# Kernel optimization log

Hardware: AMD Instinct MI355X
Metric: run time of the kernel (lower is better)

The kernel has to match this reference:

```python
import jax, jax.numpy as jnp
import numpy as np

E, C, CAP = 16, 256, 4  # experts, channels per expert, capacity expansion

def setup_inputs() -> dict:
    key = jax.random.key(0)
    k1, k2, k3, k4, k5 = jax.random.split(key, 5)
    B, L = 8, 1024
    x = jax.random.normal(k1, (B, E * C, L), dtype=jnp.float32)
    # Conv1d weights (kernel_size=1 squeezed): [out_ch, in_ch_per_group]
    W1 = jax.random.normal(k2, (E * C * CAP, C), dtype=jnp.float32) * (1.0 / np.sqrt(C))
    b1 = jax.random.normal(k3, (E * C * CAP,), dtype=jnp.float32) * 0.01
    W2 = jax.random.normal(k4, (E * C, C * CAP), dtype=jnp.float32) * (1.0 / np.sqrt(C * CAP))
    b2 = jax.random.normal(k5, (E * C,), dtype=jnp.float32) * 0.01
    return {"x": x, "W1": W1, "b1": b1, "W2": W2, "b2": b2}

def reference(x, W1, b1, W2, b2):
    # Grouped 1x1 Conv1d == block-diagonal per-expert matmul over length axis.
    B, CE, L = x.shape
    xr = x.reshape(B, E, C, L)                       # [B,E,C,L]
    W1r = W1.reshape(E, C * CAP, C)                  # [E,F,C], F = C*CAP
    W2r = W2.reshape(E, C, C * CAP)                  # [E,C,F]
    h = jnp.einsum('becl,efc->befl', xr, W1r) + b1.reshape(1, E, C * CAP, 1)
    h = jax.nn.silu(h)                               # [B,E,F,L]
    y = jnp.einsum('befl,ecf->becl', h, W2r) + b2.reshape(1, E, C, 1)
    return y.reshape(B, E * C, L)
```

## Files before the change

### kernel.cpp

```cpp
#include <hip/hip_runtime.h>
#include <hip/hip_bf16.h>
#include <stdint.h>

#define EE 16
#define CC 256
#define FF 1024
#define LL 1024
#define BB 8
#define TL 128
#define FC 32
#define NCH 32
#define HSTR 40

typedef __bf16 bf16x8 __attribute__((ext_vector_type(8)));
typedef __bf16 bf16x4 __attribute__((ext_vector_type(4)));
typedef float  f32x4  __attribute__((ext_vector_type(4)));

__device__ __forceinline__ f32x4 mfma16(bf16x8 a, bf16x8 b, f32x4 c) {
    return __builtin_amdgcn_mfma_f32_16x16x32_bf16(a, b, c, 0, 0, 0);
}

__device__ __forceinline__ void gld_lds16(const __bf16* g, __bf16* l) {
    __builtin_amdgcn_global_load_lds(
        (const __attribute__((address_space(1))) void*)g,
        (__attribute__((address_space(3))) void*)l, 16, 0, 0);
}

__global__ __launch_bounds__(256)
void cvt_both(const float* __restrict__ W1, const float* __restrict__ W2,
              __bf16* __restrict__ ws1, __bf16* __restrict__ ws2)
{
    __shared__ __align__(16) __bf16 ls[8448];
    const int t = threadIdx.x;
    const int bid = blockIdx.x;
    if (bid < 512) {
        const float* src = W1 + (size_t)bid * 8192;
        #pragma unroll
        for (int i = 0; i < 8; ++i) {
            const int p = t + 256 * i;
            const float4 v = *(const float4*)(src + 4 * p);
            const int f = p >> 6, c4 = p & 63;
            const int cg = c4 >> 1, j0 = (c4 & 1) * 4;
            bf16x4 o;
            o[0] = (__bf16)v.x; o[1] = (__bf16)v.y; o[2] = (__bf16)v.z; o[3] = (__bf16)v.w;
            *(bf16x4*)(ls + cg * 264 + f * 8 + j0) = o;
        }
        __syncthreads();
        __bf16* dst = ws1 + (size_t)bid * 8192;
        #pragma unroll
        for (int i = 0; i < 4; ++i) {
            const int G = t + 256 * i;
            const int cg = G >> 5, f = G & 31;
            *(bf16x8*)(dst + (size_t)G * 8) = *(const bf16x8*)(ls + cg * 264 + f * 8);
        }
    } else {
        const int tile = bid - 512;
        const float* src = W2 + (size_t)(tile >> 5) * 262144 + (tile & 31) * 32;
        #pragma unroll
        for (int i = 0; i < 8; ++i) {
            const int u = t + 256 * i;
            const int c = u >> 3, col4 = u & 7;
            const float4 v = *(const float4*)(src + (size_t)c * 1024 + col4 * 4);
            const int fg = col4 >> 1, j0 = (col4 & 1) * 4;
            bf16x4 o;
            o[0] = (__bf16)v.x; o[1] = (__bf16)v.y; o[2] = (__bf16)v.z; o[3] = (__bf16)v.w;
            *(bf16x4*)(ls + fg * 2056 + c * 8 + j0) = o;
        }
        __syncthreads();
        __bf16* dst = ws2 + (size_t)tile * 8192;
        #pragma unroll
        for (int i = 0; i < 4; ++i) {
            const int G = t + 256 * i;
            const int fg = G >> 8, c = G & 255;
            *(bf16x8*)(dst + (size_t)G * 8) = *(const bf16x8*)(ls + fg * 2056 + c * 8);
        }
    }
}

__global__ __launch_bounds__(1024, 4)
void experts_kernel(const float* __restrict__ x,
                    const __bf16* __restrict__ w1ws,
                    const float* __restrict__ b1,
                    const __bf16* __restrict__ w2ws,
                    const float* __restrict__ b2,
                    float* __restrict__ out)
{
    __shared__ __align__(16) __bf16 sW1[3][FC * CC];
    __shared__ __align__(16) __bf16 sW2[3][CC * FC];
    __shared__ __align__(16) __bf16 sH[2][4][32 * HSTR];

    const int tid  = threadIdx.x;
    const int lane = tid & 63;
    const int w    = tid >> 6;
    const int l15  = lane & 15, q4 = lane >> 4;
    const bool prod = (w < 8);
    const int fh   = w & 1;
    const int lw   = (w & 7) >> 1;

    const int bid  = blockIdx.x;
    const int e    = ((bid & 7) << 1) | ((bid >> 3) & 1);
    const int rest = bid >> 4;
    const int bb   = rest & 7;
    const int l0   = (rest >> 3) * TL;
    const int lb   = l0 + 32 * lw;

    const __bf16* w1c = w1ws + (size_t)e * (NCH * FC * CC);
    const __bf16* w2c = w2ws + (size_t)e * (NCH * CC * FC);
    const int slice = w * 512;

    gld_lds16(w1c + 0 * 8192 + slice + lane * 8, &sW1[0][slice]);
    gld_lds16(w2c + 0 * 8192 + slice + lane * 8, &sW2[0][slice]);
    gld_lds16(w1c + 1 * 8192 + slice + lane * 8, &sW1[1][slice]);
    gld_lds16(w2c + 1 * 8192 + slice + lane * 8, &sW2[1][slice]);

    f32x4 st[2][8];
    if (prod) {
        const float* xp = x + ((size_t)(bb * EE + e) * CC) * LL + lb + l15;
        #pragma unroll
        for (int lt = 0; lt < 2; ++lt) {
            #pragma unroll
            for (int ks = 0; ks < 8; ++ks) {
                bf16x8 f;
                #pragma unroll
                for (int u = 0; u < 8; ++u)
                    f[u] = (__bf16)xp[(size_t)(32 * ks + 8 * q4 + u) * LL + 16 * lt];
                st[lt][ks] = __builtin_bit_cast(f32x4, f);
            }
        }
    } else {
        #pragma unroll
        for (int lt = 0; lt < 2; ++lt)
            #pragma unroll
            for (int u = 0; u < 8; ++u) st[lt][u] = f32x4{0.f, 0.f, 0.f, 0.f};
    }

    __syncthreads();

    int rp = 0;
    #pragma unroll 1
    for (int ch = 0; ch <= NCH; ++ch) {
        const int rq = (rp >= 1) ? rp - 1 : 2;

        if (prod) {
            if (ch < NCH) {
                const float4 bv = *(const float4*)(b1 + e * FF + ch * FC + 16 * fh + 4 * q4);
                f32x4 a0 = f32x4{0.f, 0.f, 0.f, 0.f};
                f32x4 a1 = f32x4{0.f, 0.f, 0.f, 0.f};
                const __bf16* a1base = &sW1[rp][(16 * fh + l15) * 8];
                __builtin_amdgcn_s_setprio(1);
                #pragma unroll
                for (int ks = 0; ks < 8; ++ks) {
                    bf16x8 a = *(const bf16x8*)(a1base + (4 * ks + q4) * 256);
                    a0 = mfma16(a, __builtin_bit_cast(bf16x8, st[0][ks]), a0);
                    a1 = mfma16(a, __builtin_bit_cast(bf16x8, st[1][ks]), a1);
                }
                __builtin_amdgcn_s_setprio(0);
                __bf16* hrow = &sH[ch & 1][lw][l15 * HSTR + 16 * fh + 4 * q4];
                bf16x4 hv;
                #pragma unroll
                for (int r = 0; r < 4; ++r) {
                    float v = a0[r] + ((const float*)&bv)[r];
                    hv[r] = (__bf16)(v / (1.0f + __expf(-v)));
                }
                *(bf16x4*)hrow = hv;
                #pragma unroll
                for (int r = 0; r < 4; ++r) {
                    float v = a1[r] + ((const float*)&bv)[r];
                    hv[r] = (__bf16)(v / (1.0f + __expf(-v)));
                }
                *(bf16x4*)(hrow + 16 * HSTR) = hv;
            }
        } else if (ch >= 1) {
            const __bf16* hbase = &sH[(ch & 1) ^ 1][lw][l15 * HSTR + 8 * q4];
            bf16x8 h0 = *(const bf16x8*)(hbase);
            bf16x8 h1 = *(const bf16x8*)(hbase + 16 * HSTR);
            const __bf16* a2base = &sW2[rq][(128 * fh + l15) * 8];
            __builtin_amdgcn_s_setprio(1);
            #pragma unroll
            for (int u = 0; u < 8; ++u) {
                bf16x8 a = *(const bf16x8*)(a2base + (q4 * 256 + 16 * u) * 8);
                st[0][u] = mfma16(a, h0, st[0][u]);
                st[1][u] = mfma16(a, h1, st[1][u]);
            }
            __builtin_amdgcn_s_setprio(0);
        }

        if (ch < NCH) {
            __syncthreads();
            if (ch + 2 < NCH) {
                gld_lds16(w1c + (size_t)(ch + 2) * 8192 + slice + lane * 8, &sW1[rq][slice]);
                gld_lds16(w2c + (size_t)(ch + 2) * 8192 + slice + lane * 8, &sW2[rq][slice]);
            }
        }
        rp = (rp >= 2) ? 0 : rp + 1;
    }

    if (!prod) {
        float* outp = out + ((size_t)(bb * EE + e) * CC) * LL + lb + l15;
        #pragma unroll
        for (int u = 0; u < 8; ++u) {
            const int c0 = 128 * fh + 16 * u + 4 * q4;
            const float4 b2v = *(const float4*)(b2 + e * CC + c0);
            #pragma unroll
            for (int lt = 0; lt < 2; ++lt) {
                #pragma unroll
                for (int r = 0; r < 4; ++r)
                    __builtin_nontemporal_store(
                        st[lt][u][r] + ((const float*)&b2v)[r],
                        outp + (size_t)(c0 + r) * LL + 16 * lt);
            }
        }
    }
}

extern "C" void kernel_launch(void* const* d_in, const int* in_sizes, int n_in,
                              void* d_out, int out_size, void* d_ws, size_t ws_size,
                              hipStream_t stream)
{
    const float* x  = (const float*)d_in[0];
    const float* W1 = (const float*)d_in[1];
    const float* b1 = (const float*)d_in[2];
    const float* W2 = (const float*)d_in[3];
    const float* b2 = (const float*)d_in[4];
    float* out = (float*)d_out;

    const size_t nW1 = (size_t)EE * FF * CC;
    __bf16* w1bf = (__bf16*)d_ws;
    __bf16* w2bf = w1bf + nW1;

    cvt_both<<<dim3(1024), dim3(256), 0, stream>>>(W1, W2, w1bf, w2bf);

    experts_kernel<<<dim3(BB * EE * (LL / TL)), dim3(1024), 0, stream>>>(
        x, w1bf, b1, w2bf, b2, out);
}
```

Before: 455.4 us.

## Read expert weights directly from global memory and halve the L tile

Removes the triple-buffered LDS staging of W1/W2 chunks through global_load_lds. Each wave now loads its MFMA A-fragments straight from global memory, relying on L2 for reuse. The L tile shrinks from 128 to 64 and the block from 1024 to 512 threads, which doubles the grid and cuts LDS use to the small H exchange buffer, allowing more resident blocks. The cost is more global/L2 weight traffic per unit of work, since each block fetches the full expert weights for half as many columns, and weight-load latency is no longer hidden by prefetching. The s_setprio hint is also dropped from the first GEMM.

```diff
diff --git a/kernel.cpp b/kernel.cpp
--- a/kernel.cpp
+++ b/kernel.cpp
@@ -7,7 +7,7 @@
 #define FF 1024
 #define LL 1024
 #define BB 8
-#define TL 128
+#define TL 64
 #define FC 32
 #define NCH 32
 #define HSTR 40
@@ -18,12 +18,6 @@
 
 __device__ __forceinline__ f32x4 mfma16(bf16x8 a, bf16x8 b, f32x4 c) {
     return __builtin_amdgcn_mfma_f32_16x16x32_bf16(a, b, c, 0, 0, 0);
-}
-
-__device__ __forceinline__ void gld_lds16(const __bf16* g, __bf16* l) {
-    __builtin_amdgcn_global_load_lds(
-        (const __attribute__((address_space(1))) void*)g,
-        (__attribute__((address_space(3))) void*)l, 16, 0, 0);
 }
 
 __global__ __launch_bounds__(256)
@@ -77,7 +71,7 @@
     }
 }
 
-__global__ __launch_bounds__(1024, 4)
+__global__ __launch_bounds__(512, 4)
 void experts_kernel(const float* __restrict__ x,
                     const __bf16* __restrict__ w1ws,
                     const float* __restrict__ b1,
@@ -85,17 +79,16 @@
                     const float* __restrict__ b2,
                     float* __restrict__ out)
 {
-    __shared__ __align__(16) __bf16 sW1[3][FC * CC];
-    __shared__ __align__(16) __bf16 sW2[3][CC * FC];
-    __shared__ __align__(16) __bf16 sH[2][4][32 * HSTR];
+    __shared__ __align__(16) __bf16 sH[2][2][32 * HSTR];
 
     const int tid  = threadIdx.x;
     const int lane = tid & 63;
     const int w    = tid >> 6;
     const int l15  = lane & 15, q4 = lane >> 4;
-    const bool prod = (w < 8);
-    const int fh   = w & 1;
-    const int lw   = (w & 7) >> 1;
+    const bool prod = (w < 4);
+    const int wr   = w & 3;
+    const int fh   = wr & 1;
+    const int lw   = wr >> 1;
 
     const int bid  = blockIdx.x;
     const int e    = ((bid & 7) << 1) | ((bid >> 3) & 1);
@@ -104,14 +97,10 @@
     const int l0   = (rest >> 3) * TL;
     const int lb   = l0 + 32 * lw;
 
-    const __bf16* w1c = w1ws + (size_t)e * (NCH * FC * CC);
-    const __bf16* w2c = w2ws + (size_t)e * (NCH * CC * FC);
-    const int slice = w * 512;
-
-    gld_lds16(w1c + 0 * 8192 + slice + lane * 8, &sW1[0][slice]);
-    gld_lds16(w2c + 0 * 8192 + slice + lane * 8, &sW2[0][slice]);
-    gld_lds16(w1c + 1 * 8192 + slice + lane * 8, &sW1[1][slice]);
-    gld_lds16(w2c + 1 * 8192 + slice + lane * 8, &sW2[1][slice]);
+    const __bf16* w1p = w1ws + (size_t)e * (NCH * FC * CC)
+                      + q4 * 256 + (16 * fh + l15) * 8;
+    const __bf16* w2p = w2ws + (size_t)e * (NCH * CC * FC)
+                      + q4 * 2048 + (128 * fh + l15) * 8;
 
     f32x4 st[2][8];
     if (prod) {
@@ -134,27 +123,20 @@
             for (int u = 0; u < 8; ++u) st[lt][u] = f32x4{0.f, 0.f, 0.f, 0.f};
     }
 
-    __syncthreads();
-
-    int rp = 0;
     #pragma unroll 1
     for (int ch = 0; ch <= NCH; ++ch) {
-        const int rq = (rp >= 1) ? rp - 1 : 2;
-
         if (prod) {
             if (ch < NCH) {
                 const float4 bv = *(const float4*)(b1 + e * FF + ch * FC + 16 * fh + 4 * q4);
-                f32x4 a0 = f32x4{0.f, 0.f, 0.f, 0.f};
-                f32x4 a1 = f32x4{0.f, 0.f, 0.f, 0.f};
-                const __bf16* a1base = &sW1[rp][(16 * fh + l15) * 8];
-                __builtin_amdgcn_s_setprio(1);
+                const __bf16* wp = w1p + (size_t)ch * 8192;
+                f32x4 a0 = f32x4{0.f,0.f,0.f,0.f};
+                f32x4 a1 = f32x4{0.f,0.f,0.f,0.f};
                 #pragma unroll
                 for (int ks = 0; ks < 8; ++ks) {
-                    bf16x8 a = *(const bf16x8*)(a1base + (4 * ks + q4) * 256);
+                    bf16x8 a = *(const bf16x8*)(wp + ks * 1024);
                     a0 = mfma16(a, __builtin_bit_cast(bf16x8, st[0][ks]), a0);
                     a1 = mfma16(a, __builtin_bit_cast(bf16x8, st[1][ks]), a1);
                 }
-                __builtin_amdgcn_s_setprio(0);
                 __bf16* hrow = &sH[ch & 1][lw][l15 * HSTR + 16 * fh + 4 * q4];
                 bf16x4 hv;
                 #pragma unroll
@@ -171,28 +153,21 @@
                 *(bf16x4*)(hrow + 16 * HSTR) = hv;
             }
         } else if (ch >= 1) {
-            const __bf16* hbase = &sH[(ch & 1) ^ 1][lw][l15 * HSTR + 8 * q4];
+            const __bf16* hbase = &sH[(ch - 1) & 1][lw][l15 * HSTR + 8 * q4];
             bf16x8 h0 = *(const bf16x8*)(hbase);
             bf16x8 h1 = *(const bf16x8*)(hbase + 16 * HSTR);
-            const __bf16* a2base = &sW2[rq][(128 * fh + l15) * 8];
+            const __bf16* wp = w2p + (size_t)(ch - 1) * 8192;
             __builtin_amdgcn_s_setprio(1);
             #pragma unroll
             for (int u = 0; u < 8; ++u) {
-                bf16x8 a = *(const bf16x8*)(a2base + (q4 * 256 + 16 * u) * 8);
+                bf16x8 a = *(const bf16x8*)(wp + u * 128);
                 st[0][u] = mfma16(a, h0, st[0][u]);
                 st[1][u] = mfma16(a, h1, st[1][u]);
             }
             __builtin_amdgcn_s_setprio(0);
         }
 
-        if (ch < NCH) {
-            __syncthreads();
-            if (ch + 2 < NCH) {
-                gld_lds16(w1c + (size_t)(ch + 2) * 8192 + slice + lane * 8, &sW1[rq][slice]);
-                gld_lds16(w2c + (size_t)(ch + 2) * 8192 + slice + lane * 8, &sW2[rq][slice]);
-            }
-        }
-        rp = (rp >= 2) ? 0 : rp + 1;
+        if (ch < NCH) __syncthreads();
     }
 
     if (!prod) {
@@ -230,6 +205,6 @@
 
     cvt_both<<<dim3(1024), dim3(256), 0, stream>>>(W1, W2, w1bf, w2bf);
 
-    experts_kernel<<<dim3(BB * EE * (LL / TL)), dim3(1024), 0, stream>>>(
+    experts_kernel<<<dim3(BB * EE * (LL / TL)), dim3(512), 0, stream>>>(
         x, w1bf, b1, w2bf, b2, out);
 }
```

Measured after the change: 524.0 us. +15.1%, slower.
